# Performance work log

Hardware: AMD Instinct MI355X
Metric: run time of the kernel (lower is better)

Reference implementation:

```python
import jax, jax.numpy as jnp
import numpy as np

B, T, C, H = 4, 2048, 1024, 16
HD = C // H  # head_dim = 64


def setup_inputs() -> dict:
    key = jax.random.key(0)
    k1, k2, k3, k4, k5 = jax.random.split(key, 5)
    s = 1.0 / np.sqrt(C)
    return {
        "x": jax.random.normal(k1, (B, T, C), dtype=jnp.float32),
        "W_attn": jax.random.normal(k2, (C, 3 * C), dtype=jnp.float32) * s,
        "b_attn": jax.random.normal(k3, (3 * C,), dtype=jnp.float32) * 0.02,
        "W_proj": jax.random.normal(k4, (C, C), dtype=jnp.float32) * s,
        "b_proj": jax.random.normal(k5, (C,), dtype=jnp.float32) * 0.02,
    }


def reference(x, W_attn, b_attn, W_proj, b_proj):
    b, t, c = x.shape
    qkv = x @ W_attn + b_attn                      # [B,T,3C]
    q, k, v = jnp.split(qkv, 3, axis=-1)
    # [B,T,C] -> [B,H,T,HD]
    q = q.reshape(b, t, H, HD).transpose(0, 2, 1, 3)
    k = k.reshape(b, t, H, HD).transpose(0, 2, 1, 3)
    v = v.reshape(b, t, H, HD).transpose(0, 2, 1, 3)
    att = jnp.einsum("bhqd,bhkd->bhqk", q, k) * (1.0 / np.sqrt(HD))
    causal = jnp.tril(jnp.ones((t, t), dtype=bool))
    att = jnp.where(causal[None, None], att, -jnp.inf)
    att = jax.nn.softmax(att, axis=-1)
    y = jnp.einsum("bhqk,bhkd->bhqd", att, v)      # [B,H,T,HD]
    y = y.transpose(0, 2, 1, 3).reshape(b, t, c)
    return y @ W_proj + b_proj
```

## Files before the change

### kernel.cpp

```cpp
#include <hip/hip_runtime.h>
#include <hip/hip_bf16.h>

#define B_ 4
#define T_ 2048
#define C_ 1024
#define H_ 16
#define HD_ 64
#define M_ (B_*T_)
#define N3_ (3*C_)
#define QKVSZ (B_*H_*T_*HD_)
#define QSCALE 0.1803368801f

typedef unsigned short u16;
typedef unsigned int u32;
typedef __attribute__((ext_vector_type(8))) __bf16 bf16x8;
typedef __attribute__((ext_vector_type(4))) float f32x4;
typedef __attribute__((ext_vector_type(16))) float f32x16;
typedef __attribute__((ext_vector_type(2))) int i32x2;
typedef __attribute__((ext_vector_type(4))) u32 u32x4;
typedef const __attribute__((address_space(1))) void* gptr_t;
typedef __attribute__((address_space(3))) void* sptr_t;

__device__ __forceinline__ u16 f2b(float f) {
  __hip_bfloat16 h = __float2bfloat16(f);
  return __builtin_bit_cast(u16, h);
}

__device__ __forceinline__ u32 cvtpk(float lo, float hi) {
  u32 r;
  asm volatile("v_cvt_pk_bf16_f32 %0, %1, %2" : "=v"(r) : "v"(lo), "v"(hi));
  return r;
}

__global__ __launch_bounds__(256) void cvt_kernel(const float* __restrict__ src,
                                                  u16* __restrict__ dst, int n4) {
  int i = blockIdx.x * blockDim.x + threadIdx.x;
  int stride = gridDim.x * blockDim.x;
  for (; i < n4; i += stride) {
    float4 f = ((const float4*)src)[i];
    ushort4 o;
    o.x = f2b(f.x); o.y = f2b(f.y); o.z = f2b(f.z); o.w = f2b(f.w);
    ((ushort4*)dst)[i] = o;
  }
}

__global__ __launch_bounds__(256) void tr_cvt(const float* __restrict__ src,
                                              u16* __restrict__ dst, int K, int N) {
  __shared__ u16 tile[64][72];
  int k0 = blockIdx.x * 64, n0 = blockIdx.y * 64;
  #pragma unroll
  for (int t = 0; t < 16; ++t) {
    int idx = threadIdx.x + t * 256;
    int r = idx >> 6, c = idx & 63;
    tile[r][c] = f2b(src[(size_t)(k0 + r) * N + n0 + c]);
  }
  __syncthreads();
  #pragma unroll
  for (int t = 0; t < 16; ++t) {
    int idx = threadIdx.x + t * 256;
    int r = idx >> 6, c = idx & 63;
    dst[(size_t)(n0 + r) * K + k0 + c] = tile[c][r];
  }
}

template <int EPI>
__global__ __launch_bounds__(256, 2) void gemm_bt(const u16* __restrict__ A,
                                                  const u16* __restrict__ Bt,
                                                  const float* __restrict__ bias,
                                                  int K, int N,
                                                  u16* __restrict__ out_qkv,
                                                  float* __restrict__ out_f) {
  __shared__ __align__(16) u16 As[3][256 * 32];
  __shared__ __align__(16) u16 Bs[3][128 * 32];
  const int tid = threadIdx.x;
  const int wave = tid >> 6, lane = tid & 63;
  const int lr = lane & 15, lk = lane >> 4;

  const int m0 = blockIdx.x * 256, n0 = blockIdx.y * 128;
  const int wr = (wave >> 1) * 128, wc = (wave & 1) * 64;

  f32x4 acc[8][4] = {};

  auto stage = [&](int buf, int it) {
    const int kt = it * 32;
    #pragma unroll
    for (int i = 0; i < 4; ++i) {
      int ch = i * 256 + wave * 64 + lane;
      int row = ch >> 2;
      int gsrc = (ch & 3) ^ ((row >> 1) & 3);
      __builtin_amdgcn_global_load_lds((gptr_t)(A + (size_t)(m0 + row) * K + kt + gsrc * 8),
                                       (sptr_t)(&As[buf][ch * 8]), 16, 0, 0);
    }
    #pragma unroll
    for (int i = 0; i < 2; ++i) {
      int ch = i * 256 + wave * 64 + lane;
      int row = ch >> 2;
      int gsrc = (ch & 3) ^ ((row >> 1) & 3);
      __builtin_amdgcn_global_load_lds((gptr_t)(Bt + (size_t)(n0 + row) * K + kt + gsrc * 8),
                                       (sptr_t)(&Bs[buf][ch * 8]), 16, 0, 0);
    }
  };

  const int KI = K / 32;
  stage(0, 0);
  stage(1, 1);
  asm volatile("s_waitcnt vmcnt(6)" ::: "memory");
  __builtin_amdgcn_s_barrier();

  for (int it = 0; it < KI; ++it) {
    const int cur = it % 3;
    const bool pre = (it + 2 < KI);
    if (pre) stage((it + 2) % 3, it + 2);

    bf16x8 af[8], bfr[4];
    #pragma unroll
    for (int mi = 0; mi < 8; ++mi) {
      int r = wr + mi * 16 + lr;
      af[mi] = *(const bf16x8*)(&As[cur][r * 32 + ((lk ^ ((r >> 1) & 3)) << 3)]);
    }
    #pragma unroll
    for (int ni = 0; ni < 4; ++ni) {
      int r = wc + ni * 16 + lr;
      bfr[ni] = *(const bf16x8*)(&Bs[cur][r * 32 + ((lk ^ ((r >> 1) & 3)) << 3)]);
    }
    #pragma unroll
    for (int mi = 0; mi < 8; ++mi)
      #pragma unroll
      for (int ni = 0; ni < 4; ++ni)
        acc[mi][ni] = __builtin_amdgcn_mfma_f32_16x16x32_bf16(af[mi], bfr[ni], acc[mi][ni], 0, 0, 0);

    if (pre) asm volatile("s_waitcnt vmcnt(6)" ::: "memory");
    else     asm volatile("s_waitcnt vmcnt(0)" ::: "memory");
    __builtin_amdgcn_s_barrier();
  }

  if (EPI == 0) {
    const int sel = (n0 >> 10);
    #pragma unroll
    for (int mi = 0; mi < 8; ++mi) {
      #pragma unroll
      for (int ni = 0; ni < 4; ++ni) {
        int m = m0 + wr + mi * 16 + lk * 4;
        int n = n0 + wc + ni * 16 + lr;
        int rem = n & 1023, h = rem >> 6, d = rem & 63;
        int b = m >> 11, t = m & 2047;
        if (sel == 2) {
          ushort4 st;
          #pragma unroll
          for (int j = 0; j < 4; ++j)
            ((u16*)&st)[j] = f2b(acc[mi][ni][j] + bias[n]);
          *(ushort4*)(out_qkv + 2 * (size_t)QKVSZ +
                      (((size_t)(b * H_ + h) * HD_ + d) * T_ + t)) = st;
        } else {
          #pragma unroll
          for (int j = 0; j < 4; ++j) {
            float val = acc[mi][ni][j] + bias[n];
            if (sel == 0) val *= QSCALE;
            out_qkv[(size_t)sel * QKVSZ +
                    (((size_t)(b * H_ + h) * T_ + (t + j)) * HD_ + d)] = f2b(val);
          }
        }
      }
    }
  } else {
    #pragma unroll
    for (int mi = 0; mi < 8; ++mi)
      #pragma unroll
      for (int ni = 0; ni < 4; ++ni)
        #pragma unroll
        for (int j = 0; j < 4; ++j) {
          int m = m0 + wr + mi * 16 + lk * 4 + j;
          int n = n0 + wc + ni * 16 + lr;
          out_f[(size_t)m * C_ + n] = acc[mi][ni][j] + bias[n];
        }
  }
}

__global__ __launch_bounds__(128, 2) void attn_k(const u16* __restrict__ q,
                                                 const u16* __restrict__ k,
                                                 const u16* __restrict__ vt,
                                                 u16* __restrict__ y) {
  __shared__ __align__(16) u16 Ks[2][64 * 64];
  __shared__ __align__(16) u16 Vs[2][64 * 64];
  const int tid = threadIdx.x;
  const int wave = tid >> 6, lane = tid & 63;
  const int hi = lane >> 5, lq = lane & 31;
  const int qtb = gridDim.y - 1 - blockIdx.y;
  const int bh = blockIdx.x;
  const size_t koff = (size_t)bh * T_ * HD_;
  const size_t voff = (size_t)bh * HD_ * T_;
  const int qrow = qtb * 64 + 32 * wave + lq;

  bf16x8 qf[4];
  #pragma unroll
  for (int c = 0; c < 4; ++c)
    qf[c] = *(const bf16x8*)(q + koff + (size_t)qrow * HD_ + 16 * c + 8 * hi);

  f32x16 o[2] = {};
  float mrun = -1e30f, lsum = 0.f;

  auto stage = [&](int buf, int kt) {
    const u16* kb = k + koff + (size_t)kt * 64 * HD_;
    const u16* vb = vt + voff + (size_t)kt * 64;
    #pragma unroll
    for (int j = 0; j < 4; ++j) {
      int cb = j * 128 + wave * 64;
      int ch = cb + lane;
      int row = ch >> 3, gg = ch & 7;
      int src = gg ^ (row & 7);
      __builtin_amdgcn_global_load_lds((gptr_t)(kb + row * HD_ + src * 8),
                                       (sptr_t)(&Ks[buf][cb * 8]), 16, 0, 0);
      __builtin_amdgcn_global_load_lds((gptr_t)(vb + (size_t)row * T_ + src * 8),
                                       (sptr_t)(&Vs[buf][cb * 8]), 16, 0, 0);
    }
  };

  const int nt = qtb + 1;
  stage(0, 0);
  __syncthreads();

  for (int kt = 0; kt < nt; ++kt) {
    const int cur = kt & 1;
    if (kt + 1 < nt) stage(cur ^ 1, kt + 1);
    const bool dia = (kt == qtb);
    const bool skip1 = dia && (wave == 0);
    const u16* Kb = &Ks[cur][0];
    const u16* Vb = &Vs[cur][0];

    f32x16 s[2] = {};
    #pragma unroll
    for (int c = 0; c < 4; ++c) {
      #pragma unroll
      for (int kh = 0; kh < 2; ++kh) {
        if (kh == 1 && skip1) continue;
        int row = 32 * kh + lq;
        bf16x8 kf = *(const bf16x8*)(Kb + row * 64 + (((2 * c + hi) ^ (row & 7)) << 3));
        s[kh] = __builtin_amdgcn_mfma_f32_32x32x16_bf16(kf, qf[c], s[kh], 0, 0, 0);
      }
    }

    if (dia) {
      #pragma unroll
      for (int rr = 0; rr < 16; ++rr) {
        int kg = 64 * kt + 4 * hi + (rr & 3) + 8 * (rr >> 2);
        if (wave == 0) { if (kg > qrow) s[0][rr] = -1e30f; }
        else           { if (kg + 32 > qrow) s[1][rr] = -1e30f; }
      }
    }

    float g0, g1, g2, g3;
    {
      const f32x16& a = s[0];
      g0 = fmaxf(fmaxf(a[0], a[1]),   fmaxf(a[2], a[3]));
      g1 = fmaxf(fmaxf(a[4], a[5]),   fmaxf(a[6], a[7]));
      g2 = fmaxf(fmaxf(a[8], a[9]),   fmaxf(a[10], a[11]));
      g3 = fmaxf(fmaxf(a[12], a[13]), fmaxf(a[14], a[15]));
    }
    if (!skip1) {
      const f32x16& a = s[1];
      g0 = fmaxf(g0, fmaxf(fmaxf(a[0], a[1]),   fmaxf(a[2], a[3])));
      g1 = fmaxf(g1, fmaxf(fmaxf(a[4], a[5]),   fmaxf(a[6], a[7])));
      g2 = fmaxf(g2, fmaxf(fmaxf(a[8], a[9]),   fmaxf(a[10], a[11])));
      g3 = fmaxf(g3, fmaxf(fmaxf(a[12], a[13]), fmaxf(a[14], a[15])));
    }
    float tm = fmaxf(fmaxf(g0, g1), fmaxf(g2, g3));
    tm = fmaxf(tm, __shfl_xor(tm, 32));
    if (__any(tm > mrun + 8.f)) {
      float mn = fmaxf(mrun, tm);
      float al = __builtin_amdgcn_exp2f(mrun - mn);
      lsum *= al;
      o[0] *= al;
      o[1] *= al;
      mrun = mn;
    }
    float rs = 0.f;
    #pragma unroll
    for (int kh = 0; kh < 2; ++kh) {
      if (kh == 1 && skip1) continue;
      #pragma unroll
      for (int rr = 0; rr < 16; ++rr) {
        float p = __builtin_amdgcn_exp2f(s[kh][rr] - mrun);
        s[kh][rr] = p;
        rs += p;
      }
    }
    rs += __shfl_xor(rs, 32);
    lsum += rs;

    #pragma unroll
    for (int kh = 0; kh < 2; ++kh) {
      if (kh == 1 && skip1) continue;
      bf16x8 pf[2];
      #pragma unroll
      for (int ct = 0; ct < 2; ++ct) {
        u32 A0 = cvtpk(s[kh][8 * ct + 0], s[kh][8 * ct + 1]);
        u32 A1 = cvtpk(s[kh][8 * ct + 2], s[kh][8 * ct + 3]);
        u32 B0 = cvtpk(s[kh][8 * ct + 4], s[kh][8 * ct + 5]);
        u32 B1 = cvtpk(s[kh][8 * ct + 6], s[kh][8 * ct + 7]);
        i32x2 r0 = __builtin_amdgcn_permlane32_swap((int)A0, (int)B0, false, false);
        i32x2 r1 = __builtin_amdgcn_permlane32_swap((int)A1, (int)B1, false, false);
        u32x4 w = {(u32)r0[0], (u32)r1[0], (u32)r0[1], (u32)r1[1]};
        pf[ct] = __builtin_bit_cast(bf16x8, w);
      }
      #pragma unroll
      for (int ct = 0; ct < 2; ++ct)
        #pragma unroll
        for (int dh = 0; dh < 2; ++dh) {
          int row = 32 * dh + lq;
          bf16x8 vf = *(const bf16x8*)(Vb + row * 64 + (((4 * kh + 2 * ct + hi) ^ (row & 7)) << 3));
          o[dh] = __builtin_amdgcn_mfma_f32_32x32x16_bf16(vf, pf[ct], o[dh], 0, 0, 0);
        }
    }
    __syncthreads();
  }

  const int b = bh >> 4, h = bh & 15;
  float li = 1.0f / lsum;
  u16* yrow = y + (size_t)(b * T_ + qrow) * C_ + h * 64;
  #pragma unroll
  for (int dh = 0; dh < 2; ++dh)
    #pragma unroll
    for (int u = 0; u < 4; ++u) {
      ushort4 st;
      st.x = f2b(o[dh][4 * u + 0] * li);
      st.y = f2b(o[dh][4 * u + 1] * li);
      st.z = f2b(o[dh][4 * u + 2] * li);
      st.w = f2b(o[dh][4 * u + 3] * li);
      *(ushort4*)(yrow + 32 * dh + 8 * u + 4 * hi) = st;
    }
}

extern "C" void kernel_launch(void* const* d_in, const int* in_sizes, int n_in,
                              void* d_out, int out_size, void* d_ws, size_t ws_size,
                              hipStream_t stream) {
  const float* x      = (const float*)d_in[0];
  const float* W_attn = (const float*)d_in[1];
  const float* b_attn = (const float*)d_in[2];
  const float* W_proj = (const float*)d_in[3];
  const float* b_proj = (const float*)d_in[4];
  float* out = (float*)d_out;

  u16* ws = (u16*)d_ws;
  u16* xb  = ws;
  u16* Wat = xb + (size_t)M_ * C_;
  u16* Wpt = Wat + (size_t)N3_ * C_;
  u16* qkv = Wpt + (size_t)C_ * C_;
  u16* y   = qkv + (size_t)3 * QKVSZ;

  cvt_kernel<<<2048, 256, 0, stream>>>(x, xb, M_ * C_ / 4);
  tr_cvt<<<dim3(C_ / 64, N3_ / 64), 256, 0, stream>>>(W_attn, Wat, C_, N3_);
  tr_cvt<<<dim3(C_ / 64, C_ / 64), 256, 0, stream>>>(W_proj, Wpt, C_, C_);
  gemm_bt<0><<<dim3(M_ / 256, N3_ / 128), 256, 0, stream>>>(xb, Wat, b_attn, C_, N3_, qkv, nullptr);
  attn_k<<<dim3(B_ * H_, T_ / 64), 128, 0, stream>>>(qkv, qkv + QKVSZ, qkv + 2 * QKVSZ, y);
  gemm_bt<1><<<dim3(M_ / 256, C_ / 128), 256, 0, stream>>>(y, Wpt, b_proj, C_, C_, nullptr, out);
}
```

Before: 198.2 us.

## Split GEMM k-step into two phases interleaving loads with MFMA and priority hints

The GEMM main loop is split into two halves. Each half reads part of the A fragments, issues part of the next stage's global-to-LDS loads, passes a barrier, and then runs MFMAs at raised wave priority. This spreads memory issue across the compute and lets co-resident waves alternate between memory and math phases. s_setprio hints are also wrapped around the MFMA blocks in the attention kernel. The cost is an extra barrier per iteration, plus sched_barrier calls that constrain the compiler's scheduling.

```diff
diff --git a/kernel.cpp b/kernel.cpp
--- a/kernel.cpp
+++ b/kernel.cpp
@@ -81,11 +81,21 @@
 
   f32x4 acc[8][4] = {};
 
-  auto stage = [&](int buf, int it) {
+  auto stage_lo = [&](int buf, int it) {
     const int kt = it * 32;
     #pragma unroll
-    for (int i = 0; i < 4; ++i) {
+    for (int i = 0; i < 3; ++i) {
       int ch = i * 256 + wave * 64 + lane;
+      int row = ch >> 2;
+      int gsrc = (ch & 3) ^ ((row >> 1) & 3);
+      __builtin_amdgcn_global_load_lds((gptr_t)(A + (size_t)(m0 + row) * K + kt + gsrc * 8),
+                                       (sptr_t)(&As[buf][ch * 8]), 16, 0, 0);
+    }
+  };
+  auto stage_hi = [&](int buf, int it) {
+    const int kt = it * 32;
+    {
+      int ch = 3 * 256 + wave * 64 + lane;
       int row = ch >> 2;
       int gsrc = (ch & 3) ^ ((row >> 1) & 3);
       __builtin_amdgcn_global_load_lds((gptr_t)(A + (size_t)(m0 + row) * K + kt + gsrc * 8),
@@ -102,32 +112,55 @@
   };
 
   const int KI = K / 32;
-  stage(0, 0);
-  stage(1, 1);
+  stage_lo(0, 0); stage_hi(0, 0);
+  stage_lo(1, 1); stage_hi(1, 1);
   asm volatile("s_waitcnt vmcnt(6)" ::: "memory");
   __builtin_amdgcn_s_barrier();
 
   for (int it = 0; it < KI; ++it) {
     const int cur = it % 3;
     const bool pre = (it + 2 < KI);
-    if (pre) stage((it + 2) % 3, it + 2);
-
-    bf16x8 af[8], bfr[4];
-    #pragma unroll
-    for (int mi = 0; mi < 8; ++mi) {
-      int r = wr + mi * 16 + lr;
-      af[mi] = *(const bf16x8*)(&As[cur][r * 32 + ((lk ^ ((r >> 1) & 3)) << 3)]);
-    }
+    const int nbuf = (it + 2) % 3;
+
+    bf16x8 af0[4], af1[4], bfr[4];
     #pragma unroll
     for (int ni = 0; ni < 4; ++ni) {
       int r = wc + ni * 16 + lr;
       bfr[ni] = *(const bf16x8*)(&Bs[cur][r * 32 + ((lk ^ ((r >> 1) & 3)) << 3)]);
     }
     #pragma unroll
-    for (int mi = 0; mi < 8; ++mi)
+    for (int mi = 0; mi < 4; ++mi) {
+      int r = wr + mi * 16 + lr;
+      af0[mi] = *(const bf16x8*)(&As[cur][r * 32 + ((lk ^ ((r >> 1) & 3)) << 3)]);
+    }
+    if (pre) stage_lo(nbuf, it + 2);
+    __builtin_amdgcn_s_barrier();
+    asm volatile("s_waitcnt lgkmcnt(0)" ::: "memory");
+    __builtin_amdgcn_sched_barrier(0);
+    __builtin_amdgcn_s_setprio(1);
+    #pragma unroll
+    for (int mi = 0; mi < 4; ++mi)
       #pragma unroll
       for (int ni = 0; ni < 4; ++ni)
-        acc[mi][ni] = __builtin_amdgcn_mfma_f32_16x16x32_bf16(af[mi], bfr[ni], acc[mi][ni], 0, 0, 0);
+        acc[mi][ni] = __builtin_amdgcn_mfma_f32_16x16x32_bf16(af0[mi], bfr[ni], acc[mi][ni], 0, 0, 0);
+    __builtin_amdgcn_s_setprio(0);
+
+    #pragma unroll
+    for (int mi = 0; mi < 4; ++mi) {
+      int r = wr + 64 + mi * 16 + lr;
+      af1[mi] = *(const bf16x8*)(&As[cur][r * 32 + ((lk ^ ((r >> 1) & 3)) << 3)]);
+    }
+    if (pre) stage_hi(nbuf, it + 2);
+    __builtin_amdgcn_s_barrier();
+    asm volatile("s_waitcnt lgkmcnt(0)" ::: "memory");
+    __builtin_amdgcn_sched_barrier(0);
+    __builtin_amdgcn_s_setprio(1);
+    #pragma unroll
+    for (int mi = 0; mi < 4; ++mi)
+      #pragma unroll
+      for (int ni = 0; ni < 4; ++ni)
+        acc[mi + 4][ni] = __builtin_amdgcn_mfma_f32_16x16x32_bf16(af1[mi], bfr[ni], acc[mi + 4][ni], 0, 0, 0);
+    __builtin_amdgcn_s_setprio(0);
 
     if (pre) asm volatile("s_waitcnt vmcnt(6)" ::: "memory");
     else     asm volatile("s_waitcnt vmcnt(0)" ::: "memory");
@@ -228,6 +261,7 @@
     const u16* Vb = &Vs[cur][0];
 
     f32x16 s[2] = {};
+    __builtin_amdgcn_s_setprio(1);
     #pragma unroll
     for (int c = 0; c < 4; ++c) {
       #pragma unroll
@@ -238,6 +272,7 @@
         s[kh] = __builtin_amdgcn_mfma_f32_32x32x16_bf16(kf, qf[c], s[kh], 0, 0, 0);
       }
     }
+    __builtin_amdgcn_s_setprio(0);
 
     if (dia) {
       #pragma unroll
@@ -302,6 +337,7 @@
         u32x4 w = {(u32)r0[0], (u32)r1[0], (u32)r0[1], (u32)r1[1]};
         pf[ct] = __builtin_bit_cast(bf16x8, w);
       }
+      __builtin_amdgcn_s_setprio(1);
       #pragma unroll
       for (int ct = 0; ct < 2; ++ct)
         #pragma unroll
@@ -310,6 +346,7 @@
           bf16x8 vf = *(const bf16x8*)(Vb + row * 64 + (((4 * kh + 2 * ct + hi) ^ (row & 7)) << 3));
           o[dh] = __builtin_amdgcn_mfma_f32_32x32x16_bf16(vf, pf[ct], o[dh], 0, 0, 0);
         }
+      __builtin_amdgcn_s_setprio(0);
     }
     __syncthreads();
   }
```

New measurement: 182.3 us. -8.0%, faster.
